# Kernel optimization log

Measured on AMD Instinct MI355X. Metric: run time of the kernel, lower is better.

The kernel has to match this reference:

```python
import jax, jax.numpy as jnp
import numpy as np

B, C_IN, C_OUT, H, W = 4, 64, 64, 128, 128
N = 9  # 3x3 sampling points


def setup_inputs() -> dict:
    key = jax.random.key(0)
    k1, k2, k3, k4 = jax.random.split(key, 4)
    x = jax.random.normal(k1, (B, C_IN, H, W), jnp.float32)
    alpha = jax.random.normal(k2, (B, 1, H, W), jnp.float32)
    # kaiming_uniform(a=sqrt(5)) on (C_OUT, C_IN, 3, 3): bound = 1/sqrt(fan_in)
    fan_in = C_IN * 9
    bound = 1.0 / np.sqrt(fan_in)
    weight = jax.random.uniform(k3, (C_OUT, C_IN, 3, 3), jnp.float32, -bound, bound)
    bias = jax.random.uniform(k4, (C_OUT,), jnp.float32, -bound, bound)
    return {"x": x, "alpha": alpha, "weight": weight, "bias": bias}


def _forward(x, alpha, weight, bias):
    b, c, h, w = x.shape
    xp = jnp.pad(x, ((0, 0), (0, 0), (1, 1), (1, 1)))  # ZeroPad2d(1)
    hp, wp = h + 2, w + 2
    dt = x.dtype

    # kernel offsets, N index n = kx*3 + ky (kx slow)
    ks = jnp.arange(-1, 2, dtype=dt)
    pnx = jnp.repeat(ks, 3)  # [-1,-1,-1,0,0,0,1,1,1]
    pny = jnp.tile(ks, 3)    # [-1,0,1,-1,0,1,-1,0,1]

    cosA = jnp.cos(alpha)  # (b,1,h,w)
    sinA = jnp.sin(alpha)
    p0x = jnp.arange(1, h + 1, dtype=dt)[:, None]  # (h,1)
    p0y = jnp.arange(1, w + 1, dtype=dt)[None, :]  # (1,w)
    # note: original code multiplies each coord by (cos +/- sin) of alpha
    px = pnx[None, :, None, None] * (cosA + sinA) + p0x[None, None]  # (b,9,h,w)
    py = pny[None, :, None, None] * (cosA - sinA) + p0y[None, None]
    px = jnp.moveaxis(px, 1, -1)  # (b,h,w,9)
    py = jnp.moveaxis(py, 1, -1)

    fx, fy = jnp.floor(px), jnp.floor(py)  # detached in original (floor grad = 0)
    qx0 = jnp.clip(fx, 0, hp - 1)
    qx1 = jnp.clip(fx + 1, 0, hp - 1)
    qy0 = jnp.clip(fy, 0, wp - 1)
    qy1 = jnp.clip(fy + 1, 0, wp - 1)

    g_lt = (1 + (qx0 - px)) * (1 + (qy0 - py))
    g_rb = (1 - (qx1 - px)) * (1 - (qy1 - py))
    g_lb = (1 + (qx0 - px)) * (1 - (qy1 - py))
    g_rt = (1 - (qx1 - px)) * (1 + (qy0 - py))

    xf = xp.reshape(b, c, hp * wp)
    ix0, ix1 = qx0.astype(jnp.int32), qx1.astype(jnp.int32)
    iy0, iy1 = qy0.astype(jnp.int32), qy1.astype(jnp.int32)

    def gather(ix, iy):
        idx = (ix * wp + iy).reshape(b, -1)  # row-major flatten, like torch gather
        v = jax.vmap(lambda xb, ib: xb[:, ib])(xf, idx)  # (b,c,h*w*9)
        return v.reshape(b, c, h, w, N)

    emap = (g_lt[:, None] * gather(ix0, iy0)
            + g_rb[:, None] * gather(ix1, iy1)
            + g_lb[:, None] * gather(ix0, iy1)
            + g_rt[:, None] * gather(ix1, iy0))  # (b,c,h,w,9)

    # _reshape_x_offset: out[b,c, i*3+ky, j*3+kx] = emap[b,c,i,j, kx*3+ky]
    e = emap.reshape(b, c, h, w, 3, 3)              # (...,kx,ky)
    e = e.transpose(0, 1, 2, 5, 3, 4).reshape(b, c, 3 * h, 3 * w)

    # Dconv: central-difference weights, middle row = -(top + bottom)
    o, i = weight.shape[0], weight.shape[1]
    wr = weight.reshape(o, i, 9)
    r0, r2 = wr[:, :, 0:3], wr[:, :, 6:9]
    buf = jnp.concatenate([r0, -r0 - r2, r2], axis=-1).reshape(o, i, 3, 3)

    y = jax.lax.conv_general_dilated(
        e, buf, window_strides=(3, 3), padding='VALID',
        dimension_numbers=('NCHW', 'OIHW', 'NCHW'))
    return y + bias[None, :, None, None]


def reference(x, alpha, weight, bias):
    return _forward(x, alpha, weight, bias)
```

## Files before the change

### kernel.cpp

```cpp
#include <hip/hip_runtime.h>

#define CIN  64
#define COUT 64
#define Hn   128
#define Wn   128
#define HW   (Hn * Wn)
#define KDIM 576
#define WROW 1152
#define EROW 640

#define NRQ 8
#define NCQ 12
#define NCHUNKQ (NRQ * NCQ * 8)
#define PIXB 144
#define TILE_BYTES (NRQ * NCQ * PIXB)

typedef __attribute__((ext_vector_type(8))) short bf16x8;
typedef __attribute__((ext_vector_type(4))) float f32x4;
typedef __attribute__((ext_vector_type(2))) float f32x2;

__device__ __forceinline__ unsigned short f2bf(float f) {
    unsigned u = __float_as_uint(f);
    unsigned r = u + 0x7FFFu + ((u >> 16) & 1u);
    return (unsigned short)(r >> 16);
}
__device__ __forceinline__ unsigned pk2c(float a, float b) {
    unsigned r;
    asm("v_cvt_pk_bf16_f32 %0, %1, %2" : "=v"(r) : "v"(a), "v"(b));
    return r;
}


__global__ __launch_bounds__(256) void prep_fused(
    const float* __restrict__ x, const float* __restrict__ weight,
    unsigned short* __restrict__ xt, unsigned short* __restrict__ Wtb2)
{
    __shared__ float fbuf[64][65];
    if (blockIdx.x >= 1024) {
        int e = (blockIdx.x - 1024) * 256 + threadIdx.x;
        if (e < COUT * KDIM) {
            int o = e / KDIM, k = e % KDIM;
            int n = k >> 6, c = k & 63;
            int u = n % 3, v = n / 3;
            float w0 = weight[((o * CIN + c) * 3 + 0) * 3 + v];
            float w2 = weight[((o * CIN + c) * 3 + 2) * 3 + v];
            float val = (u == 0) ? w0 : ((u == 1) ? (-w0 - w2) : w2);
            int s = c >> 5;
            int ce = c & 31;
            Wtb2[((n * 2 + s) * 64 + o) * 32 + ce] = f2bf(val);
        }
        return;
    }
    const int blk = blockIdx.x;
    const int b   = blk >> 8;
    const int rem = blk & 255;
    const int h   = rem >> 1;
    const int w0  = (rem & 1) << 6;
    const int t   = threadIdx.x;
    {
        int wq = t & 63, cq = t >> 6;
        const float* xp = x + ((size_t)(b * CIN + cq * 16) * Hn + h) * Wn + w0 + wq;
        #pragma unroll
        for (int r = 0; r < 16; ++r)
            fbuf[wq][cq * 16 + r] = xp[(size_t)r * HW];
    }
    __syncthreads();
    {
        int wq = t >> 2, q = t & 3;
        const float* row = &fbuf[wq][q * 16];
        uint4 d0, d1;
        d0.x = pk2c(row[0],  row[1]);  d0.y = pk2c(row[2],  row[3]);
        d0.z = pk2c(row[4],  row[5]);  d0.w = pk2c(row[6],  row[7]);
        d1.x = pk2c(row[8],  row[9]);  d1.y = pk2c(row[10], row[11]);
        d1.z = pk2c(row[12], row[13]); d1.w = pk2c(row[14], row[15]);
        unsigned short* op = xt + ((size_t)(b * Hn + h) * Wn + w0 + wq) * 64 + q * 16;
        *reinterpret_cast<uint4*>(op)     = d0;
        *reinterpret_cast<uint4*>(op + 8) = d1;
    }
}

template<int D>
__device__ __forceinline__ void axis_pts(float s, int base1, int org,
                                         int& l0, int& l1, float& w0, float& w1)
{
    float p  = (float)D * s + (float)base1;
    float f  = floorf(p);
    float q0 = fminf(fmaxf(f,       0.f), 129.f);
    float q1 = fminf(fmaxf(f + 1.f, 0.f), 129.f);
    w0 = 1.f + (q0 - p);  w1 = 1.f - (q1 - p);
    int i0 = (int)q0, i1 = (int)q1;
    if (i0 < 1 || i0 > 128) w0 = 0.f;
    if (i1 < 1 || i1 > 128) w1 = 0.f;
    l0 = min(max(i0 - 1, 0), 127) - org;
    l1 = min(max(i1 - 1, 0), 127) - org;
}

__device__ __forceinline__ unsigned pixb(int lr, int lc, int g16) {
    return (unsigned)((lr * NCQ + lc) * PIXB + g16);
}

template<int DXc, int DYc, int EDX, int EDY>
__device__ __forceinline__ void geoW(float s1, float s2, int ipx, int iorg,
        int jpx, int jorg, int g16, unsigned A[4], float AG[4],
        unsigned B[2], float BG[2])
{
    int r0, r1, c0, c1; float wx0, wx1, wy0, wy1;
    axis_pts<DXc>(s1, ipx + 1, iorg, r0, r1, wx0, wx1);
    axis_pts<DYc>(s2, jpx + 1, jorg, c0, c1, wy0, wy1);
    A[0] = pixb(r0, c0, g16);  AG[0] = wx0 * wy0;
    A[1] = pixb(r0, c1, g16);  AG[1] = wx0 * wy1;
    A[2] = pixb(r1, c0, g16);  AG[2] = wx1 * wy0;
    A[3] = pixb(r1, c1, g16);  AG[3] = wx1 * wy1;
    if (EDY == 0) {
        int lc = jpx - jorg;
        B[0] = pixb(r0, lc, g16);  BG[0] = wx0;
        B[1] = pixb(r1, lc, g16);  BG[1] = wx1;
    } else if (EDY == DYc) {
        int lr = ipx - iorg;
        B[0] = pixb(lr, c0, g16);  BG[0] = wy0;
        B[1] = pixb(lr, c1, g16);  BG[1] = wy1;
    } else {
        int e0, e1; float v0, v1;
        axis_pts<EDY>(s2, jpx + 1, jorg, e0, e1, v0, v1);
        int lr = ipx - iorg;
        B[0] = pixb(lr, e0, g16);  BG[0] = v0;
        B[1] = pixb(lr, e1, g16);  BG[1] = v1;
    }
}

__device__ __forceinline__ f32x2 bfpair(unsigned u) {
    f32x2 r;
    r.x = __uint_as_float(u << 16);
    r.y = __uint_as_float(u & 0xFFFF0000u);
    return r;
}

__device__ __forceinline__ void fma16p(uint4 rl, uint4 rh, float gw,
                                       f32x2* v0, f32x2* v1) {
    const unsigned* u0 = reinterpret_cast<const unsigned*>(&rl);
    const unsigned* u1 = reinterpret_cast<const unsigned*>(&rh);
    f32x2 g2; g2.x = gw; g2.y = gw;
    #pragma unroll
    for (int q = 0; q < 4; ++q) {
        v0[q] = __builtin_elementwise_fma(g2, bfpair(u0[q]), v0[q]);
        v1[q] = __builtin_elementwise_fma(g2, bfpair(u1[q]), v1[q]);
    }
}

__device__ __forceinline__ bf16x8 packv2(const f32x2* v) {
    uint4 p;
    p.x = pk2c(v[0].x, v[0].y); p.y = pk2c(v[1].x, v[1].y);
    p.z = pk2c(v[2].x, v[2].y); p.w = pk2c(v[3].x, v[3].y);
    union { uint4 u; bf16x8 b; } cv; cv.u = p;
    return cv.b;
}

__global__ __launch_bounds__(256, 3) void ddconv_ws3(
    const unsigned short* __restrict__ xt, const float* __restrict__ alpha,
    const unsigned short* __restrict__ Wtb2, const float* __restrict__ bias,
    float* __restrict__ out)
{
    __shared__ __align__(16) char smem[40960];

    const int blk  = ((blockIdx.x & 7) << 8) + (blockIdx.x >> 3);
    const int b    = blk >> 9;
    const int rem  = blk & 511;
    const int i0   = (rem >> 4) << 2;
    const int j0   = (rem & 15) << 3;
    const int t    = threadIdx.x;
    const int lane = t & 63;
    const int w    = t >> 6;
    const int llo  = lane & 15;
    const int g    = lane >> 4;
    const int g16  = g * 16;
    const int iorg = i0 - 2, jorg = j0 - 2;

    const char* xtb = (const char*)xt + (size_t)b * HW * 128;
    const char* wt2 = (const char*)Wtb2;
    const int arow  = llo * 64 + g16;

    char* tile = smem;
    uint4    sv[3];
    unsigned sla[3];
    {
        const char* sgp[3];
        const int slot16 = (t & 7) << 4;
        #pragma unroll
        for (int k = 0; k < 3; ++k) {
            int q  = t + k * 256;
            int rc = q >> 3;
            int row = rc / NCQ;
            int col = rc - row * NCQ;
            int ru  = min(max(iorg + row, 0), 127);
            int cu  = min(max(jorg + col, 0), 127);
            sgp[k] = xtb + (size_t)(((ru << 7) + cu) << 7) + slot16;
            sla[k] = (unsigned)(rc * PIXB) + slot16;
        }
        #pragma unroll
        for (int k = 0; k < 3; ++k)
            sv[k] = *reinterpret_cast<const uint4*>(sgp[k]);
    }
    #pragma unroll
    for (int k = 0; k < 3; ++k)
        *reinterpret_cast<uint4*>(tile + sla[k]) = sv[k];

    const int nn0 = (w==0)?0:(w==1)?2:(w==2)?6:8;
    const int nn1 = (w==0)?1:(w==1)?3:(w==2)?7:5;
    const int cs  = w >> 1;
    bf16x8 Ata[2][4], Atb[2][4], Ac0, Ac1;
    #pragma unroll
    for (int s = 0; s < 2; ++s)
      #pragma unroll
      for (int ot = 0; ot < 4; ++ot) {
        Ata[s][ot] = *reinterpret_cast<const bf16x8*>(wt2 + (nn0*2+s)*4096 + ot*1024 + arow);
        Atb[s][ot] = *reinterpret_cast<const bf16x8*>(wt2 + (nn1*2+s)*4096 + ot*1024 + arow);
      }
    Ac0 = *reinterpret_cast<const bf16x8*>(wt2 + (8+cs)*4096 + ((w&1)*2  )*1024 + arow);
    Ac1 = *reinterpret_cast<const bf16x8*>(wt2 + (8+cs)*4096 + ((w&1)*2+1)*1024 + arow);

    float* sAB = reinterpret_cast<float*>(smem + TILE_BYTES);
    if (t < 32) {
        float a = alpha[(b * Hn + i0 + (t >> 3)) * Wn + j0 + (t & 7)];
        float sa, ca;
        sincosf(a, &sa, &ca);
        sAB[t]      = ca + sa;
        sAB[32 + t] = ca - sa;
    }

    f32x4 acc[2][4];
    #pragma unroll
    for (int pg = 0; pg < 2; ++pg)
      #pragma unroll
      for (int ot = 0; ot < 4; ++ot) acc[pg][ot] = (f32x4){0.f, 0.f, 0.f, 0.f};

    __syncthreads();

    float S1[2], S2[2];
    #pragma unroll
    for (int pg = 0; pg < 2; ++pg) {
        S1[pg] = sAB[pg * 16 + llo];
        S2[pg] = sAB[32 + pg * 16 + llo];
    }

    #define LDT(o) (*reinterpret_cast<const uint4*>(tile + (o)))

    #pragma unroll
    for (int pg = 0; pg < 2; ++pg) {
        const int ipx = i0 + pg * 2 + (llo >> 3);
        const int jpx = j0 + (llo & 7);

        unsigned A[4], B[2];
        float    AG[4], BG[2];
        if (w == 0) {
            geoW<-1,-1,-1, 0>(S1[pg], S2[pg], ipx, iorg, jpx, jorg, g16, A, AG, B, BG);
        } else if (w == 1) {
            geoW<-1, 1, 0,-1>(S1[pg], S2[pg], ipx, iorg, jpx, jorg, g16, A, AG, B, BG);
        } else if (w == 2) {
            geoW< 1,-1, 1, 0>(S1[pg], S2[pg], ipx, iorg, jpx, jorg, g16, A, AG, B, BG);
        } else {
            geoW< 1, 1, 0, 1>(S1[pg], S2[pg], ipx, iorg, jpx, jorg, g16, A, AG, B, BG);
        }
        unsigned cAddr = pixb(ipx - iorg, jpx - jorg, g16) + (cs ? 64u : 0u);

        uint4 La[4], Ha[4];
        #pragma unroll
        for (int p = 0; p < 4; ++p) {
            La[p] = LDT(A[p]);
            Ha[p] = LDT(A[p] + 64);
        }
        uint4 Lb[2], Hb[2];
        #pragma unroll
        for (int p = 0; p < 2; ++p) {
            Lb[p] = LDT(B[p]);
            Hb[p] = LDT(B[p] + 64);
        }
        bf16x8 bc;
        {
            union { uint4 u; bf16x8 b; } cv; cv.u = LDT(cAddr); bc = cv.b;
        }

        f32x2 v0[4], v1[4];
        #pragma unroll
        for (int q = 0; q < 4; ++q) { v0[q] = (f32x2){0.f,0.f}; v1[q] = (f32x2){0.f,0.f}; }
        #pragma unroll
        for (int p = 0; p < 4; ++p) fma16p(La[p], Ha[p], AG[p], v0, v1);
        bf16x8 bA0 = packv2(v0), bA1 = packv2(v1);

        f32x2 u0[4], u1[4];
        #pragma unroll
        for (int q = 0; q < 4; ++q) { u0[q] = (f32x2){0.f,0.f}; u1[q] = (f32x2){0.f,0.f}; }
        #pragma unroll
        for (int p = 0; p < 2; ++p) fma16p(Lb[p], Hb[p], BG[p], u0, u1);
        bf16x8 bB0 = packv2(u0), bB1 = packv2(u1);

        #pragma unroll
        for (int ot = 0; ot < 4; ++ot) {
            acc[pg][ot] = __builtin_amdgcn_mfma_f32_16x16x32_bf16(Ata[0][ot], bA0, acc[pg][ot], 0, 0, 0);
            acc[pg][ot] = __builtin_amdgcn_mfma_f32_16x16x32_bf16(Ata[1][ot], bA1, acc[pg][ot], 0, 0, 0);
            acc[pg][ot] = __builtin_amdgcn_mfma_f32_16x16x32_bf16(Atb[0][ot], bB0, acc[pg][ot], 0, 0, 0);
            acc[pg][ot] = __builtin_amdgcn_mfma_f32_16x16x32_bf16(Atb[1][ot], bB1, acc[pg][ot], 0, 0, 0);
        }
        if (w & 1) {
            acc[pg][2] = __builtin_amdgcn_mfma_f32_16x16x32_bf16(Ac0, bc, acc[pg][2], 0, 0, 0);
            acc[pg][3] = __builtin_amdgcn_mfma_f32_16x16x32_bf16(Ac1, bc, acc[pg][3], 0, 0, 0);
        } else {
            acc[pg][0] = __builtin_amdgcn_mfma_f32_16x16x32_bf16(Ac0, bc, acc[pg][0], 0, 0, 0);
            acc[pg][1] = __builtin_amdgcn_mfma_f32_16x16x32_bf16(Ac1, bc, acc[pg][1], 0, 0, 0);
        }
    }
    #undef LDT

    __syncthreads();
    #pragma unroll
    for (int pg = 0; pg < 2; ++pg)
      #pragma unroll
      for (int ot = 0; ot < 4; ++ot)
        *reinterpret_cast<f32x4*>(smem + ((pg*256 + w*64 + lane)*80) + ot*16) = acc[pg][ot];
    __syncthreads();
    {
        const int eq = w;
        #pragma unroll
        for (int pg = 0; pg < 2; ++pg) {
            f32x4 s = (f32x4){0.f, 0.f, 0.f, 0.f};
            #pragma unroll
            for (int ww = 0; ww < 4; ++ww)
                s += *reinterpret_cast<const f32x4*>(smem + ((pg*256 + ww*64 + lane)*80) + eq*16);
            float* ob = out + (size_t)b * COUT * HW
                      + (size_t)(i0 + pg * 2 + (llo >> 3)) * Wn + j0 + (llo & 7);
            #pragma unroll
            for (int r = 0; r < 4; ++r) {
                int o = eq * 16 + g * 4 + r;
                ob[(size_t)o * HW] = s[r] + bias[o];
            }
        }
    }
}


__device__ __forceinline__ unsigned pk2f(float a, float b) {
    return (unsigned)f2bf(a) | ((unsigned)f2bf(b) << 16);
}

__global__ void prep_weights(const float* __restrict__ weight,
                             unsigned short* __restrict__ Wtb) {
    int e = blockIdx.x * 256 + threadIdx.x;
    if (e >= COUT * KDIM) return;
    int o = e / KDIM, k = e % KDIM;
    int n = k >> 6, c = k & 63;
    int u = n % 3, v = n / 3;
    float w0 = weight[((o * CIN + c) * 3 + 0) * 3 + v];
    float w2 = weight[((o * CIN + c) * 3 + 2) * 3 + v];
    float val = (u == 0) ? w0 : ((u == 1) ? (-w0 - w2) : w2);
    Wtb[o * KDIM + k] = f2bf(val);
}

template<int DX, int DY>
__device__ __forceinline__ void gatherG(const float* __restrict__ xb,
    float s1, float s2, int i, int jj, int klocal,
    char* myrow, unsigned swz, int c0s, int c1s)
{
    int ix0 = 0, ix1 = 0; float wx0 = 1.f, wx1 = 0.f;
    if (DX != 0) {
        float px = (float)DX * s1 + (float)(i + 1);
        float fx = floorf(px);
        float qx0 = fminf(fmaxf(fx, 0.f), 129.f);
        float qx1 = fminf(fmaxf(fx + 1.f, 0.f), 129.f);
        wx0 = 1.f + (qx0 - px); wx1 = 1.f - (qx1 - px);
        ix0 = (int)qx0; ix1 = (int)qx1;
    } else { ix0 = i + 1; }
    int iy0 = 0, iy1 = 0; float wy0 = 1.f, wy1 = 0.f;
    if (DY != 0) {
        float py = (float)DY * s2 + (float)(jj + 1);
        float fy = floorf(py);
        float qy0 = fminf(fmaxf(fy, 0.f), 129.f);
        float qy1 = fminf(fmaxf(fy + 1.f, 0.f), 129.f);
        wy0 = 1.f + (qy0 - py); wy1 = 1.f - (qy1 - py);
        iy0 = (int)qy0; iy1 = (int)qy1;
    } else { iy0 = jj + 1; }

    constexpr int NX = (DX ? 2 : 1), NY = (DY ? 2 : 1), NT = NX * NY;
    unsigned idx[NT]; float g[NT];
    const int   ixs[2] = { ix0, ix1 };  const float wxs[2] = { wx0, wx1 };
    const int   iys[2] = { iy0, iy1 };  const float wys[2] = { wy0, wy1 };
    #pragma unroll
    for (int xi = 0; xi < NX; ++xi)
      #pragma unroll
      for (int yi = 0; yi < NY; ++yi) {
        int ix = ixs[xi], iy = iys[yi];
        bool ok = (ix >= 1) && (ix <= Hn) && (iy >= 1) && (iy <= Wn);
        int cx = min(max(ix, 1), Hn) - 1;
        int cy = min(max(iy, 1), Wn) - 1;
        idx[xi * NY + yi] = (unsigned)(cx * Wn + cy);
        g[xi * NY + yi]   = ok ? wxs[xi] * wys[yi] : 0.f;
      }
    for (int c0 = c0s; c0 < c1s; c0 += 8) {
        float v[8];
        #pragma unroll
        for (int cc = 0; cc < 8; ++cc) {
            unsigned coff = (unsigned)(c0 + cc) * HW;
            float acc2 = 0.f;
            #pragma unroll
            for (int tp = 0; tp < NT; ++tp)
                acc2 = fmaf(g[tp], xb[coff + idx[tp]], acc2);
            v[cc] = acc2;
        }
        uint4 d;
        d.x = pk2f(v[0], v[1]); d.y = pk2f(v[2], v[3]);
        d.z = pk2f(v[4], v[5]); d.w = pk2f(v[6], v[7]);
        unsigned addr = (unsigned)(klocal + c0) * 2u;
        *reinterpret_cast<uint4*>(myrow + (addr ^ swz)) = d;
    }
}

template<int KS>
__device__ __forceinline__ void mfma_phase(const char* emap,
    const unsigned short* __restrict__ Wtb,
    int w, int lane, int passbyte, f32x4 acc[4])
{
    const int llo = lane & 15, lhi = lane >> 4;
    const unsigned prow = (unsigned)(w * 16 + llo);
    const unsigned psw  = (prow & 7u) << 4;
    const char* erow = emap + prow * EROW;
    const char* wtb  = (const char*)Wtb + passbyte + lhi * 16;
    #pragma unroll
    for (int s = 0; s < KS; ++s) {
        unsigned kb = (unsigned)(s * 64 + lhi * 16);
        bf16x8 bf = *reinterpret_cast<const bf16x8*>(erow + (kb ^ psw));
        #pragma unroll
        for (int ot = 0; ot < 4; ++ot) {
            const char* ap = wtb + (ot * 16 + llo) * WROW + s * 64;
            bf16x8 af = *reinterpret_cast<const bf16x8*>(ap);
            acc[ot] = __builtin_amdgcn_mfma_f32_16x16x32_bf16(af, bf, acc[ot], 0, 0, 0);
        }
    }
}

__global__ __launch_bounds__(256, 3) void ddconv_mfma(
    const float* __restrict__ x, const float* __restrict__ alpha,
    const unsigned short* __restrict__ Wtb, const float* __restrict__ bias,
    float* __restrict__ out)
{
    __shared__ __align__(16) char emap[64 * EROW];
    const int blk  = blockIdx.x;
    const int b    = blk >> 8;
    const int rem  = blk & 255;
    const int i    = rem >> 1;
    const int j0   = (rem & 1) << 6;
    const int t    = threadIdx.x;
    const int lane = t & 63;
    const int w    = t >> 6;
    const int jj   = j0 + lane;
    const float* xb = x + (size_t)b * CIN * HW;
    float a = alpha[(b * Hn + i) * Wn + jj];
    float sa, ca;
    sincosf(a, &sa, &ca);
    const float s1 = ca + sa, s2 = ca - sa;
    char* myrow = emap + lane * EROW;
    const unsigned swz = (unsigned)((lane & 7) << 4);
    f32x4 acc[4];
    #pragma unroll
    for (int ot = 0; ot < 4; ++ot) acc[ot] = (f32x4){0.f, 0.f, 0.f, 0.f};
    if (w == 0)      { gatherG<-1,-1>(xb, s1, s2, i, jj,   0, myrow, swz,  0, 48); }
    else if (w == 1) { gatherG<-1,-1>(xb, s1, s2, i, jj,   0, myrow, swz, 48, 64);
                       gatherG<-1, 0>(xb, s1, s2, i, jj,  64, myrow, swz,  0, 64); }
    else if (w == 2) { gatherG<-1, 1>(xb, s1, s2, i, jj, 128, myrow, swz,  0, 48); }
    else             { gatherG<-1, 1>(xb, s1, s2, i, jj, 128, myrow, swz, 48, 64);
                       gatherG< 0,-1>(xb, s1, s2, i, jj, 192, myrow, swz,  0, 64); }
    __syncthreads();
    mfma_phase<8>(emap, Wtb, w, lane, 0, acc);
    __syncthreads();
    if (w == 0)      { gatherG< 1,-1>(xb, s1, s2, i, jj, 128, myrow, swz,  0, 56); }
    else if (w == 1) { gatherG< 1,-1>(xb, s1, s2, i, jj, 128, myrow, swz, 56, 64);
                       gatherG< 1, 1>(xb, s1, s2, i, jj, 256, myrow, swz,  0, 48); }
    else if (w == 2) { gatherG< 1, 1>(xb, s1, s2, i, jj, 256, myrow, swz, 48, 64);
                       gatherG< 0, 1>(xb, s1, s2, i, jj,  64, myrow, swz,  0, 64); }
    else             { gatherG< 1, 0>(xb, s1, s2, i, jj, 192, myrow, swz,  0, 64);
                       gatherG< 0, 0>(xb, s1, s2, i, jj,   0, myrow, swz,  0, 64); }
    __syncthreads();
    mfma_phase<10>(emap, Wtb, w, lane, 512, acc);
    const int llo = lane & 15, lhi = lane >> 4;
    float* ob = out + (size_t)b * COUT * HW + (size_t)i * Wn + j0 + w * 16 + llo;
    #pragma unroll
    for (int ot = 0; ot < 4; ++ot)
      #pragma unroll
      for (int r = 0; r < 4; ++r) {
        int o = ot * 16 + lhi * 4 + r;
        ob[(size_t)o * HW] = acc[ot][r] + bias[o];
      }
}


extern "C" void kernel_launch(void* const* d_in, const int* in_sizes, int n_in,
                              void* d_out, int out_size, void* d_ws, size_t ws_size,
                              hipStream_t stream) {
    const float* x      = (const float*)d_in[0];
    const float* alpha  = (const float*)d_in[1];
    const float* weight = (const float*)d_in[2];
    const float* bias   = (const float*)d_in[3];
    float* out = (float*)d_out;

    const size_t WT_BYTES = (size_t)COUT * KDIM * 2;
    const size_t XT_BYTES = (size_t)4 * HW * CIN * 2;

    if (ws_size >= WT_BYTES + XT_BYTES) {
        unsigned short* Wtb2 = (unsigned short*)d_ws;
        unsigned short* xt   = (unsigned short*)((char*)d_ws + WT_BYTES);
        prep_fused<<<1168, 256, 0, stream>>>(x, weight, xt, Wtb2);
        ddconv_ws3<<<4 * (Hn / 4) * (Wn / 8), 256, 0, stream>>>(xt, alpha, Wtb2, bias, out);
    } else {
        unsigned short* Wtb = (unsigned short*)d_ws;
        prep_weights<<<(COUT * KDIM + 255) / 256, 256, 0, stream>>>(weight, Wtb);
        ddconv_mfma<<<4 * Hn * (Wn / 64), 256, 0, stream>>>(x, alpha, Wtb, bias, out);
    }
}
```

Before: 32.38 us.

## Double block tile width to reuse halo and weights across two subtiles

Each block now covers a 4x16 pixel tile instead of 4x8 and processes it as two 8-wide subtiles. The halo tile grows to 8x20 pixels, loaded with 5 vector loads per thread, so the halo overhead per output pixel drops and the register-resident weight fragments are reused twice. The grid is halved, and the block-index swizzle across batches is removed in favour of a linear order. The cross-wave reduction now runs per subtile and per pixel group through a dedicated shared buffer, which adds extra barriers, and the larger shared footprint may reduce occupancy.

```diff
diff --git a/kernel.cpp b/kernel.cpp
--- a/kernel.cpp
+++ b/kernel.cpp
@@ -10,10 +10,13 @@
 #define EROW 640
 
 #define NRQ 8
-#define NCQ 12
+#define NCQ 20
 #define NCHUNKQ (NRQ * NCQ * 8)
 #define PIXB 144
 #define TILE_BYTES (NRQ * NCQ * PIXB)
+#define SAB_OFF  TILE_BYTES
+#define RED_OFF  (TILE_BYTES + 512)
+#define SMEM_BYTES (RED_OFF + 20480)
 
 typedef __attribute__((ext_vector_type(8))) short bf16x8;
 typedef __attribute__((ext_vector_type(4))) float f32x4;
@@ -160,13 +163,13 @@
     const unsigned short* __restrict__ Wtb2, const float* __restrict__ bias,
     float* __restrict__ out)
 {
-    __shared__ __align__(16) char smem[40960];
-
-    const int blk  = ((blockIdx.x & 7) << 8) + (blockIdx.x >> 3);
-    const int b    = blk >> 9;
-    const int rem  = blk & 511;
-    const int i0   = (rem >> 4) << 2;
-    const int j0   = (rem & 15) << 3;
+    __shared__ __align__(16) char smem[SMEM_BYTES];
+
+    const int blk  = blockIdx.x;
+    const int b    = blk >> 8;
+    const int rem  = blk & 255;
+    const int i0   = (rem >> 3) << 2;
+    const int j0   = (rem & 7) << 4;
     const int t    = threadIdx.x;
     const int lane = t & 63;
     const int w    = t >> 6;
@@ -180,13 +183,13 @@
     const int arow  = llo * 64 + g16;
 
     char* tile = smem;
-    uint4    sv[3];
-    unsigned sla[3];
+    uint4    sv[5];
+    unsigned sla[5];
     {
-        const char* sgp[3];
+        const char* sgp[5];
         const int slot16 = (t & 7) << 4;
         #pragma unroll
-        for (int k = 0; k < 3; ++k) {
+        for (int k = 0; k < 5; ++k) {
             int q  = t + k * 256;
             int rc = q >> 3;
             int row = rc / NCQ;
@@ -197,11 +200,11 @@
             sla[k] = (unsigned)(rc * PIXB) + slot16;
         }
         #pragma unroll
-        for (int k = 0; k < 3; ++k)
+        for (int k = 0; k < 5; ++k)
             sv[k] = *reinterpret_cast<const uint4*>(sgp[k]);
     }
     #pragma unroll
-    for (int k = 0; k < 3; ++k)
+    for (int k = 0; k < 5; ++k)
         *reinterpret_cast<uint4*>(tile + sla[k]) = sv[k];
 
     const int nn0 = (w==0)?0:(w==1)?2:(w==2)?6:8;
@@ -218,115 +221,118 @@
     Ac0 = *reinterpret_cast<const bf16x8*>(wt2 + (8+cs)*4096 + ((w&1)*2  )*1024 + arow);
     Ac1 = *reinterpret_cast<const bf16x8*>(wt2 + (8+cs)*4096 + ((w&1)*2+1)*1024 + arow);
 
-    float* sAB = reinterpret_cast<float*>(smem + TILE_BYTES);
-    if (t < 32) {
-        float a = alpha[(b * Hn + i0 + (t >> 3)) * Wn + j0 + (t & 7)];
+    float* sAB = reinterpret_cast<float*>(smem + SAB_OFF);
+    if (t < 64) {
+        int row = i0 + ((t >> 4) & 1) * 2 + ((t >> 3) & 1);
+        int col = j0 + (t >> 5) * 8 + (t & 7);
+        float a = alpha[(b * Hn + row) * Wn + col];
         float sa, ca;
         sincosf(a, &sa, &ca);
         sAB[t]      = ca + sa;
-        sAB[32 + t] = ca - sa;
-    }
-
-    f32x4 acc[2][4];
-    #pragma unroll
-    for (int pg = 0; pg < 2; ++pg)
+        sAB[64 + t] = ca - sa;
+    }
+
+    __syncthreads();
+
+    float S1[2][2], S2[2][2];
+    #pragma unroll
+    for (int st = 0; st < 2; ++st)
       #pragma unroll
-      for (int ot = 0; ot < 4; ++ot) acc[pg][ot] = (f32x4){0.f, 0.f, 0.f, 0.f};
-
-    __syncthreads();
-
-    float S1[2], S2[2];
-    #pragma unroll
-    for (int pg = 0; pg < 2; ++pg) {
-        S1[pg] = sAB[pg * 16 + llo];
-        S2[pg] = sAB[32 + pg * 16 + llo];
-    }
+      for (int pg = 0; pg < 2; ++pg) {
+        S1[st][pg] = sAB[st * 32 + pg * 16 + llo];
+        S2[st][pg] = sAB[64 + st * 32 + pg * 16 + llo];
+      }
 
     #define LDT(o) (*reinterpret_cast<const uint4*>(tile + (o)))
-
-    #pragma unroll
-    for (int pg = 0; pg < 2; ++pg) {
-        const int ipx = i0 + pg * 2 + (llo >> 3);
-        const int jpx = j0 + (llo & 7);
-
-        unsigned A[4], B[2];
-        float    AG[4], BG[2];
-        if (w == 0) {
-            geoW<-1,-1,-1, 0>(S1[pg], S2[pg], ipx, iorg, jpx, jorg, g16, A, AG, B, BG);
-        } else if (w == 1) {
-            geoW<-1, 1, 0,-1>(S1[pg], S2[pg], ipx, iorg, jpx, jorg, g16, A, AG, B, BG);
-        } else if (w == 2) {
-            geoW< 1,-1, 1, 0>(S1[pg], S2[pg], ipx, iorg, jpx, jorg, g16, A, AG, B, BG);
-        } else {
-            geoW< 1, 1, 0, 1>(S1[pg], S2[pg], ipx, iorg, jpx, jorg, g16, A, AG, B, BG);
+    char* red = smem + RED_OFF;
+
+    #pragma unroll
+    for (int st = 0; st < 2; ++st) {
+        f32x4 acc[2][4];
+        #pragma unroll
+        for (int pg = 0; pg < 2; ++pg)
+          #pragma unroll
+          for (int ot = 0; ot < 4; ++ot) acc[pg][ot] = (f32x4){0.f, 0.f, 0.f, 0.f};
+
+        #pragma unroll
+        for (int pg = 0; pg < 2; ++pg) {
+            const int ipx = i0 + pg * 2 + (llo >> 3);
+            const int jpx = j0 + st * 8 + (llo & 7);
+
+            unsigned A[4], B[2];
+            float    AG[4], BG[2];
+            if (w == 0) {
+                geoW<-1,-1,-1, 0>(S1[st][pg], S2[st][pg], ipx, iorg, jpx, jorg, g16, A, AG, B, BG);
+            } else if (w == 1) {
+                geoW<-1, 1, 0,-1>(S1[st][pg], S2[st][pg], ipx, iorg, jpx, jorg, g16, A, AG, B, BG);
+            } else if (w == 2) {
+                geoW< 1,-1, 1, 0>(S1[st][pg], S2[st][pg], ipx, iorg, jpx, jorg, g16, A, AG, B, BG);
+            } else {
+                geoW< 1, 1, 0, 1>(S1[st][pg], S2[st][pg], ipx, iorg, jpx, jorg, g16, A, AG, B, BG);
+            }
+            unsigned cAddr = pixb(ipx - iorg, jpx - jorg, g16) + (cs ? 64u : 0u);
+
+            uint4 La[4], Ha[4];
+            #pragma unroll
+            for (int p = 0; p < 4; ++p) {
+                La[p] = LDT(A[p]);
+                Ha[p] = LDT(A[p] + 64);
+            }
+            uint4 Lb[2], Hb[2];
+            #pragma unroll
+            for (int p = 0; p < 2; ++p) {
+                Lb[p] = LDT(B[p]);
+                Hb[p] = LDT(B[p] + 64);
+            }
+            bf16x8 bc;
+            {
+                union { uint4 u; bf16x8 b2; } cv; cv.u = LDT(cAddr); bc = cv.b2;
+            }
+
+            f32x2 v0[4], v1[4];
+            #pragma unroll
+            for (int q = 0; q < 4; ++q) { v0[q] = (f32x2){0.f,0.f}; v1[q] = (f32x2){0.f,0.f}; }
+            #pragma unroll
+            for (int p = 0; p < 4; ++p) fma16p(La[p], Ha[p], AG[p], v0, v1);
+            bf16x8 bA0 = packv2(v0), bA1 = packv2(v1);
+
+            f32x2 u0[4], u1[4];
+            #pragma unroll
+            for (int q = 0; q < 4; ++q) { u0[q] = (f32x2){0.f,0.f}; u1[q] = (f32x2){0.f,0.f}; }
+            #pragma unroll
+            for (int p = 0; p < 2; ++p) fma16p(Lb[p], Hb[p], BG[p], u0, u1);
+            bf16x8 bB0 = packv2(u0), bB1 = packv2(u1);
+
+            #pragma unroll
+            for (int ot = 0; ot < 4; ++ot) {
+                acc[pg][ot] = __builtin_amdgcn_mfma_f32_16x16x32_bf16(Ata[0][ot], bA0, acc[pg][ot], 0, 0, 0);
+                acc[pg][ot] = __builtin_amdgcn_mfma_f32_16x16x32_bf16(Ata[1][ot], bA1, acc[pg][ot], 0, 0, 0);
+                acc[pg][ot] = __builtin_amdgcn_mfma_f32_16x16x32_bf16(Atb[0][ot], bB0, acc[pg][ot], 0, 0, 0);
+                acc[pg][ot] = __builtin_amdgcn_mfma_f32_16x16x32_bf16(Atb[1][ot], bB1, acc[pg][ot], 0, 0, 0);
+            }
+            if (w & 1) {
+                acc[pg][2] = __builtin_amdgcn_mfma_f32_16x16x32_bf16(Ac0, bc, acc[pg][2], 0, 0, 0);
+                acc[pg][3] = __builtin_amdgcn_mfma_f32_16x16x32_bf16(Ac1, bc, acc[pg][3], 0, 0, 0);
+            } else {
+                acc[pg][0] = __builtin_amdgcn_mfma_f32_16x16x32_bf16(Ac0, bc, acc[pg][0], 0, 0, 0);
+                acc[pg][1] = __builtin_amdgcn_mfma_f32_16x16x32_bf16(Ac1, bc, acc[pg][1], 0, 0, 0);
+            }
         }
-        unsigned cAddr = pixb(ipx - iorg, jpx - jorg, g16) + (cs ? 64u : 0u);
-
-        uint4 La[4], Ha[4];
-        #pragma unroll
-        for (int p = 0; p < 4; ++p) {
-            La[p] = LDT(A[p]);
-            Ha[p] = LDT(A[p] + 64);
-        }
-        uint4 Lb[2], Hb[2];
-        #pragma unroll
-        for (int p = 0; p < 2; ++p) {
-            Lb[p] = LDT(B[p]);
-            Hb[p] = LDT(B[p] + 64);
-        }
-        bf16x8 bc;
-        {
-            union { uint4 u; bf16x8 b; } cv; cv.u = LDT(cAddr); bc = cv.b;
-        }
-
-        f32x2 v0[4], v1[4];
-        #pragma unroll
-        for (int q = 0; q < 4; ++q) { v0[q] = (f32x2){0.f,0.f}; v1[q] = (f32x2){0.f,0.f}; }
-        #pragma unroll
-        for (int p = 0; p < 4; ++p) fma16p(La[p], Ha[p], AG[p], v0, v1);
-        bf16x8 bA0 = packv2(v0), bA1 = packv2(v1);
-
-        f32x2 u0[4], u1[4];
-        #pragma unroll
-        for (int q = 0; q < 4; ++q) { u0[q] = (f32x2){0.f,0.f}; u1[q] = (f32x2){0.f,0.f}; }
-        #pragma unroll
-        for (int p = 0; p < 2; ++p) fma16p(Lb[p], Hb[p], BG[p], u0, u1);
-        bf16x8 bB0 = packv2(u0), bB1 = packv2(u1);
-
-        #pragma unroll
-        for (int ot = 0; ot < 4; ++ot) {
-            acc[pg][ot] = __builtin_amdgcn_mfma_f32_16x16x32_bf16(Ata[0][ot], bA0, acc[pg][ot], 0, 0, 0);
-            acc[pg][ot] = __builtin_amdgcn_mfma_f32_16x16x32_bf16(Ata[1][ot], bA1, acc[pg][ot], 0, 0, 0);
-            acc[pg][ot] = __builtin_amdgcn_mfma_f32_16x16x32_bf16(Atb[0][ot], bB0, acc[pg][ot], 0, 0, 0);
-            acc[pg][ot] = __builtin_amdgcn_mfma_f32_16x16x32_bf16(Atb[1][ot], bB1, acc[pg][ot], 0, 0, 0);
-        }
-        if (w & 1) {
-            acc[pg][2] = __builtin_amdgcn_mfma_f32_16x16x32_bf16(Ac0, bc, acc[pg][2], 0, 0, 0);
-            acc[pg][3] = __builtin_amdgcn_mfma_f32_16x16x32_bf16(Ac1, bc, acc[pg][3], 0, 0, 0);
-        } else {
-            acc[pg][0] = __builtin_amdgcn_mfma_f32_16x16x32_bf16(Ac0, bc, acc[pg][0], 0, 0, 0);
-            acc[pg][1] = __builtin_amdgcn_mfma_f32_16x16x32_bf16(Ac1, bc, acc[pg][1], 0, 0, 0);
-        }
-    }
-    #undef LDT
-
-    __syncthreads();
-    #pragma unroll
-    for (int pg = 0; pg < 2; ++pg)
-      #pragma unroll
-      for (int ot = 0; ot < 4; ++ot)
-        *reinterpret_cast<f32x4*>(smem + ((pg*256 + w*64 + lane)*80) + ot*16) = acc[pg][ot];
-    __syncthreads();
-    {
-        const int eq = w;
+
         #pragma unroll
         for (int pg = 0; pg < 2; ++pg) {
+            __syncthreads();
+            #pragma unroll
+            for (int ot = 0; ot < 4; ++ot)
+                *reinterpret_cast<f32x4*>(red + ((w*64 + lane)*80) + ot*16) = acc[pg][ot];
+            __syncthreads();
+            const int eq = w;
             f32x4 s = (f32x4){0.f, 0.f, 0.f, 0.f};
             #pragma unroll
             for (int ww = 0; ww < 4; ++ww)
-                s += *reinterpret_cast<const f32x4*>(smem + ((pg*256 + ww*64 + lane)*80) + eq*16);
+                s += *reinterpret_cast<const f32x4*>(red + ((ww*64 + lane)*80) + eq*16);
             float* ob = out + (size_t)b * COUT * HW
-                      + (size_t)(i0 + pg * 2 + (llo >> 3)) * Wn + j0 + (llo & 7);
+                      + (size_t)(i0 + pg * 2 + (llo >> 3)) * Wn + j0 + st * 8 + (llo & 7);
             #pragma unroll
             for (int r = 0; r < 4; ++r) {
                 int o = eq * 16 + g * 4 + r;
@@ -334,6 +340,7 @@
             }
         }
     }
+    #undef LDT
 }
 
 
@@ -506,7 +513,7 @@
         unsigned short* Wtb2 = (unsigned short*)d_ws;
         unsigned short* xt   = (unsigned short*)((char*)d_ws + WT_BYTES);
         prep_fused<<<1168, 256, 0, stream>>>(x, weight, xt, Wtb2);
-        ddconv_ws3<<<4 * (Hn / 4) * (Wn / 8), 256, 0, stream>>>(xt, alpha, Wtb2, bias, out);
+        ddconv_ws3<<<4 * (Hn / 4) * (Wn / 16), 256, 0, stream>>>(xt, alpha, Wtb2, bias, out);
     } else {
         unsigned short* Wtb = (unsigned short*)d_ws;
         prep_weights<<<(COUT * KDIM + 255) / 256, 256, 0, stream>>>(weight, Wtb);
```

New measurement: 31.93 us, median of 3. Within noise of the previous version (-1.4%).
